# Kernel optimization log

Hardware: AMD Instinct MI355X
Metric: run time of the kernel (lower is better)

The kernel has to match this reference:

```python
import jax, jax.numpy as jnp
import numpy as np

LOG_2PI = float(np.log(2.0 * np.pi))
EPS = 1e-18


def setup_inputs() -> dict:
    key = jax.random.key(0)
    k1, k2, k3 = jax.random.split(key, 3)
    N_U, N_L, NZ = 4096, 65536, 32
    return {
        "pred": jax.random.normal(k1, (N_U,), dtype=jnp.float32),
        "U_z": jax.random.normal(k2, (N_U, NZ), dtype=jnp.float32),
        "L_z": jax.random.normal(k3, (N_L, NZ), dtype=jnp.float32),
    }


def reference(pred, U_z, L_z):
    # pred is accepted but unused by the original forward.
    nz = U_z.shape[1]
    # density: standard multivariate normal log-prob, mean 0, cov I
    dens = -0.5 * jnp.sum(U_z * U_z, axis=-1) - 0.5 * nz * LOG_2PI  # [N_U]
    # diversity: min_{z' in L_z} ||z - z'||_2 for each row of U_z
    # squared-distance expansion: ||u||^2 + ||l||^2 - 2 u.l
    u_sq = jnp.sum(U_z * U_z, axis=1)[:, None]        # [N_U, 1]
    l_sq = jnp.sum(L_z * L_z, axis=1)[None, :]        # [1, N_L]
    sq = u_sq + l_sq - 2.0 * (U_z @ L_z.T)            # [N_U, N_L]
    dists = jnp.sqrt(jnp.maximum(sq, 0.0))
    div = jnp.min(dists, axis=1)                      # [N_U]
    dd = jnp.exp(dens + jnp.log(div + EPS))
    dd = dd - jnp.min(dd)
    dd = dd / (jnp.max(dd) + EPS)
    return dd
```

## Files before the change

### kernel.cpp

```cpp
#include <hip/hip_runtime.h>
#include <hip/hip_bf16.h>

typedef _Float16 half8 __attribute__((ext_vector_type(8)));
typedef float f32x4 __attribute__((ext_vector_type(4)));
typedef unsigned int u32x4 __attribute__((ext_vector_type(4)));

#define N_U      4096
#define N_L      65536
#define NZ       32
#define NSPLIT   256
#define LSLICE   (N_L / NSPLIT)
#define NT       (LSLICE / 16)
#define UT       16
#define BM       1024
#define GY       (N_U / BM)

#define OFF_P1   0
#define OFF_USQ  (16 * 1024)
#define OFF_LF   (32 * 1024)
#define OFF_LSQ  (OFF_LF + N_L * NZ * 2)
#define OFF_UF   (OFF_LSQ + N_L * 4)

__device__ __forceinline__ unsigned int f2key(float f) {
    unsigned int u = __float_as_uint(f);
    return (u & 0x80000000u) ? ~u : (u | 0x80000000u);
}
__device__ __forceinline__ float key2f(unsigned int k) {
    unsigned int u = (k & 0x80000000u) ? (k & 0x7FFFFFFFu) : ~k;
    return __uint_as_float(u);
}

__global__ __launch_bounds__(256) void kPre(const float* __restrict__ Uz,
                                            const float* __restrict__ Lz,
                                            _Float16* __restrict__ Lf16,
                                            float* __restrict__ lsqh,
                                            _Float16* __restrict__ Uf16,
                                            float* __restrict__ usq,
                                            unsigned int* __restrict__ P1key) {
    int r = blockIdx.x * 256 + threadIdx.x;
    if (r < N_L) {
        const f32x4* src = (const f32x4*)(Lz + (size_t)r * NZ);
        _Float16* dst = Lf16 + (size_t)r * NZ;
        float s = 0.f;
#pragma unroll
        for (int j = 0; j < 4; ++j) {
            f32x4 a = src[2 * j], b = src[2 * j + 1];
            s = fmaf(a[0], a[0], s); s = fmaf(a[1], a[1], s);
            s = fmaf(a[2], a[2], s); s = fmaf(a[3], a[3], s);
            s = fmaf(b[0], b[0], s); s = fmaf(b[1], b[1], s);
            s = fmaf(b[2], b[2], s); s = fmaf(b[3], b[3], s);
            *(half8*)(dst + j * 8) =
                (half8){(_Float16)a[0], (_Float16)a[1], (_Float16)a[2], (_Float16)a[3],
                        (_Float16)b[0], (_Float16)b[1], (_Float16)b[2], (_Float16)b[3]};
        }
        lsqh[r] = -0.5f * s;
    } else if (r < N_L + N_U) {
        int u = r - N_L;
        const f32x4* src = (const f32x4*)(Uz + (size_t)u * NZ);
        _Float16* dst = Uf16 + (size_t)u * NZ;
        float s = 0.f;
#pragma unroll
        for (int j = 0; j < 4; ++j) {
            f32x4 a = src[2 * j], b = src[2 * j + 1];
            s = fmaf(a[0], a[0], s); s = fmaf(a[1], a[1], s);
            s = fmaf(a[2], a[2], s); s = fmaf(a[3], a[3], s);
            s = fmaf(b[0], b[0], s); s = fmaf(b[1], b[1], s);
            s = fmaf(b[2], b[2], s); s = fmaf(b[3], b[3], s);
            *(half8*)(dst + j * 8) =
                (half8){(_Float16)a[0], (_Float16)a[1], (_Float16)a[2], (_Float16)a[3],
                        (_Float16)b[0], (_Float16)b[1], (_Float16)b[2], (_Float16)b[3]};
        }
        usq[u] = s;
        P1key[u] = 0u;
    }
}

__global__ __launch_bounds__(256)
__attribute__((amdgpu_waves_per_eu(4, 4)))
void kA(const _Float16* __restrict__ Lf16,
        const float* __restrict__ lsqh,
        const _Float16* __restrict__ Uf16,
        unsigned int* __restrict__ P1key) {
    __shared__ __align__(16) unsigned char sm[LSLICE * 64 + LSLICE * 4];
    float* slsq = (float*)(sm + LSLICE * 64);

    const int tid  = threadIdx.x;
    const int lane = tid & 63;
    const int wave = tid >> 6;
    const int g    = lane >> 4;
    const int lc   = lane & 15;

    const int ubase = blockIdx.y * BM + wave * (UT * 16);
    const int lbase = blockIdx.x * LSLICE;

    {
        const half8* src = (const half8*)(Lf16 + (size_t)(lbase + tid) * NZ);
        unsigned char* dst = sm + ((tid >> 4) * 1024) + ((tid & 15) * 16);
#pragma unroll
        for (int j = 0; j < 4; ++j)
            *(half8*)(dst + j * 256) = src[j];
        slsq[tid] = lsqh[lbase + tid];
    }

    half8 bfrag[UT];
#pragma unroll
    for (int t = 0; t < UT; ++t)
        bfrag[t] = *(const half8*)(Uf16 + (size_t)(ubase + t * 16 + lc) * NZ + g * 8);
#pragma unroll
    for (int t = 0; t < UT; ++t)
        asm volatile("" : "+v"(bfrag[t]));

    float m[UT];
#pragma unroll
    for (int t = 0; t < UT; ++t) m[t] = -INFINITY;

    __syncthreads();

    const unsigned char* abase = sm + lane * 16;

#pragma unroll 2
    for (int lt = 0; lt < NT; ++lt) {
        const int pt = (lt + wave * 4) & (NT - 1);
        half8 a = *(const half8*)(abase + pt * 1024);
        f32x4 c = *(const f32x4*)(slsq + pt * 16 + g * 4);
#pragma unroll
        for (int t = 0; t < UT; ++t) {
            f32x4 x = __builtin_amdgcn_mfma_f32_16x16x32_f16(a, bfrag[t], c, 0, 0, 0);
            asm volatile("" : "+v"(x));
            float y = fmaxf(fmaxf(x[0], x[1]), x[2]);
            m[t] = fmaxf(fmaxf(y, x[3]), m[t]);
        }
    }

#pragma unroll
    for (int t = 0; t < UT; ++t) {
        float v = m[t];
        v = fmaxf(v, __shfl_xor(v, 16));
        v = fmaxf(v, __shfl_xor(v, 32));
        if (g == 0)
            atomicMax(&P1key[ubase + t * 16 + lc], f2key(v));
    }
}

__global__ __launch_bounds__(1024) void kB(const unsigned int* __restrict__ P1key,
                                           const float* __restrict__ usq,
                                           float* __restrict__ out) {
    const int t    = threadIdx.x;
    const int lane = t & 63;
    const int wid  = t >> 6;

    u32x4 kv = ((const u32x4*)P1key)[t];
    f32x4 uq = ((const f32x4*)usq)[t];

    float dd[4], lmin = INFINITY, lmax = -INFINITY;
#pragma unroll
    for (int j = 0; j < 4; ++j) {
        float M   = key2f(kv[j]);
        float sq  = fmaxf(fmaf(-2.f, M, uq[j]), 0.f);
        float dens = -0.5f * uq[j] - 29.406033062549525f;
        dd[j] = expf(dens) * (sqrtf(sq) + 1e-18f);
        lmin = fminf(lmin, dd[j]);
        lmax = fmaxf(lmax, dd[j]);
    }

    __shared__ float smn[16], smx[16];
#pragma unroll
    for (int o = 1; o < 64; o <<= 1) {
        lmin = fminf(lmin, __shfl_xor(lmin, o));
        lmax = fmaxf(lmax, __shfl_xor(lmax, o));
    }
    if (lane == 0) { smn[wid] = lmin; smx[wid] = lmax; }
    __syncthreads();
    if (wid == 0) {
        float a = (lane < 16) ? smn[lane] : INFINITY;
        float b = (lane < 16) ? smx[lane] : -INFINITY;
#pragma unroll
        for (int o = 1; o < 16; o <<= 1) {
            a = fminf(a, __shfl_xor(a, o));
            b = fmaxf(b, __shfl_xor(b, o));
        }
        if (lane == 0) { smn[0] = a; smx[0] = b; }
    }
    __syncthreads();
    float mn = smn[0], mx = smx[0];
    float inv = 1.f / ((mx - mn) + 1e-18f);

    f32x4 o4 = (f32x4){(dd[0] - mn) * inv, (dd[1] - mn) * inv,
                       (dd[2] - mn) * inv, (dd[3] - mn) * inv};
    ((f32x4*)out)[t] = o4;
}

extern "C" void kernel_launch(void* const* d_in, const int* in_sizes, int n_in,
                              void* d_out, int out_size, void* d_ws, size_t ws_size,
                              hipStream_t stream) {
    const float* Uz = (const float*)d_in[1];
    const float* Lz = (const float*)d_in[2];
    float* out = (float*)d_out;
    unsigned char* ws = (unsigned char*)d_ws;

    unsigned int* P1key = (unsigned int*)(ws + OFF_P1);
    float*        usq   = (float*)(ws + OFF_USQ);
    _Float16*     Lf16  = (_Float16*)(ws + OFF_LF);
    float*        lsqh  = (float*)(ws + OFF_LSQ);
    _Float16*     Uf16  = (_Float16*)(ws + OFF_UF);

    kPre<<<(N_L + N_U + 255) / 256, 256, 0, stream>>>(Uz, Lz, Lf16, lsqh, Uf16, usq, P1key);
    dim3 grid(NSPLIT, GY);
    kA<<<grid, 256, 0, stream>>>(Lf16, lsqh, Uf16, P1key);
    kB<<<1, 1024, 0, stream>>>(P1key, usq, out);
}
```

Measured before the change: 35.05 us.

## Fuse fp16 conversion and norm precompute into distance and finalize kernels

Removes the separate preprocessing kernel and performs the fp32-to-fp16 conversion and squared-norm computation of L rows inside the main MFMA kernel's shared-memory staging. U fragments are converted on load, and the finalize kernel recomputes U norms from the fp32 input. A memset replaces the key initialization. This saves one launch and the workspace round trip, in exchange for reading fp32 L from global memory in each of the 4 row-block groups and doing redundant conversion work.

```diff
diff --git a/kernel.cpp b/kernel.cpp
--- a/kernel.cpp
+++ b/kernel.cpp
@@ -16,10 +16,6 @@
 #define GY       (N_U / BM)
 
 #define OFF_P1   0
-#define OFF_USQ  (16 * 1024)
-#define OFF_LF   (32 * 1024)
-#define OFF_LSQ  (OFF_LF + N_L * NZ * 2)
-#define OFF_UF   (OFF_LSQ + N_L * 4)
 
 __device__ __forceinline__ unsigned int f2key(float f) {
     unsigned int u = __float_as_uint(f);
@@ -30,56 +26,10 @@
     return __uint_as_float(u);
 }
 
-__global__ __launch_bounds__(256) void kPre(const float* __restrict__ Uz,
-                                            const float* __restrict__ Lz,
-                                            _Float16* __restrict__ Lf16,
-                                            float* __restrict__ lsqh,
-                                            _Float16* __restrict__ Uf16,
-                                            float* __restrict__ usq,
-                                            unsigned int* __restrict__ P1key) {
-    int r = blockIdx.x * 256 + threadIdx.x;
-    if (r < N_L) {
-        const f32x4* src = (const f32x4*)(Lz + (size_t)r * NZ);
-        _Float16* dst = Lf16 + (size_t)r * NZ;
-        float s = 0.f;
-#pragma unroll
-        for (int j = 0; j < 4; ++j) {
-            f32x4 a = src[2 * j], b = src[2 * j + 1];
-            s = fmaf(a[0], a[0], s); s = fmaf(a[1], a[1], s);
-            s = fmaf(a[2], a[2], s); s = fmaf(a[3], a[3], s);
-            s = fmaf(b[0], b[0], s); s = fmaf(b[1], b[1], s);
-            s = fmaf(b[2], b[2], s); s = fmaf(b[3], b[3], s);
-            *(half8*)(dst + j * 8) =
-                (half8){(_Float16)a[0], (_Float16)a[1], (_Float16)a[2], (_Float16)a[3],
-                        (_Float16)b[0], (_Float16)b[1], (_Float16)b[2], (_Float16)b[3]};
-        }
-        lsqh[r] = -0.5f * s;
-    } else if (r < N_L + N_U) {
-        int u = r - N_L;
-        const f32x4* src = (const f32x4*)(Uz + (size_t)u * NZ);
-        _Float16* dst = Uf16 + (size_t)u * NZ;
-        float s = 0.f;
-#pragma unroll
-        for (int j = 0; j < 4; ++j) {
-            f32x4 a = src[2 * j], b = src[2 * j + 1];
-            s = fmaf(a[0], a[0], s); s = fmaf(a[1], a[1], s);
-            s = fmaf(a[2], a[2], s); s = fmaf(a[3], a[3], s);
-            s = fmaf(b[0], b[0], s); s = fmaf(b[1], b[1], s);
-            s = fmaf(b[2], b[2], s); s = fmaf(b[3], b[3], s);
-            *(half8*)(dst + j * 8) =
-                (half8){(_Float16)a[0], (_Float16)a[1], (_Float16)a[2], (_Float16)a[3],
-                        (_Float16)b[0], (_Float16)b[1], (_Float16)b[2], (_Float16)b[3]};
-        }
-        usq[u] = s;
-        P1key[u] = 0u;
-    }
-}
-
 __global__ __launch_bounds__(256)
 __attribute__((amdgpu_waves_per_eu(4, 4)))
-void kA(const _Float16* __restrict__ Lf16,
-        const float* __restrict__ lsqh,
-        const _Float16* __restrict__ Uf16,
+void kA(const float* __restrict__ Lz,
+        const float* __restrict__ Uz,
         unsigned int* __restrict__ P1key) {
     __shared__ __align__(16) unsigned char sm[LSLICE * 64 + LSLICE * 4];
     float* slsq = (float*)(sm + LSLICE * 64);
@@ -94,18 +44,31 @@
     const int lbase = blockIdx.x * LSLICE;
 
     {
-        const half8* src = (const half8*)(Lf16 + (size_t)(lbase + tid) * NZ);
+        const f32x4* src = (const f32x4*)(Lz + (size_t)(lbase + tid) * NZ);
         unsigned char* dst = sm + ((tid >> 4) * 1024) + ((tid & 15) * 16);
+        float s = 0.f;
 #pragma unroll
-        for (int j = 0; j < 4; ++j)
-            *(half8*)(dst + j * 256) = src[j];
-        slsq[tid] = lsqh[lbase + tid];
+        for (int j = 0; j < 4; ++j) {
+            f32x4 a = src[2 * j], b = src[2 * j + 1];
+            s = fmaf(a[0], a[0], s); s = fmaf(a[1], a[1], s);
+            s = fmaf(a[2], a[2], s); s = fmaf(a[3], a[3], s);
+            s = fmaf(b[0], b[0], s); s = fmaf(b[1], b[1], s);
+            s = fmaf(b[2], b[2], s); s = fmaf(b[3], b[3], s);
+            *(half8*)(dst + j * 256) =
+                (half8){(_Float16)a[0], (_Float16)a[1], (_Float16)a[2], (_Float16)a[3],
+                        (_Float16)b[0], (_Float16)b[1], (_Float16)b[2], (_Float16)b[3]};
+        }
+        slsq[tid] = -0.5f * s;
     }
 
     half8 bfrag[UT];
 #pragma unroll
-    for (int t = 0; t < UT; ++t)
-        bfrag[t] = *(const half8*)(Uf16 + (size_t)(ubase + t * 16 + lc) * NZ + g * 8);
+    for (int t = 0; t < UT; ++t) {
+        const f32x4* p = (const f32x4*)(Uz + (size_t)(ubase + t * 16 + lc) * NZ + g * 8);
+        f32x4 a = p[0], b = p[1];
+        bfrag[t] = (half8){(_Float16)a[0], (_Float16)a[1], (_Float16)a[2], (_Float16)a[3],
+                           (_Float16)b[0], (_Float16)b[1], (_Float16)b[2], (_Float16)b[3]};
+    }
 #pragma unroll
     for (int t = 0; t < UT; ++t)
         asm volatile("" : "+v"(bfrag[t]));
@@ -143,21 +106,29 @@
 }
 
 __global__ __launch_bounds__(1024) void kB(const unsigned int* __restrict__ P1key,
-                                           const float* __restrict__ usq,
+                                           const float* __restrict__ Uz,
                                            float* __restrict__ out) {
     const int t    = threadIdx.x;
     const int lane = t & 63;
     const int wid  = t >> 6;
 
     u32x4 kv = ((const u32x4*)P1key)[t];
-    f32x4 uq = ((const f32x4*)usq)[t];
 
     float dd[4], lmin = INFINITY, lmax = -INFINITY;
 #pragma unroll
     for (int j = 0; j < 4; ++j) {
+        const int u = t * 4 + j;
+        const f32x4* p = (const f32x4*)(Uz + (size_t)u * NZ);
+        float s = 0.f;
+#pragma unroll
+        for (int q = 0; q < 8; ++q) {
+            f32x4 v = p[q];
+            s = fmaf(v[0], v[0], s); s = fmaf(v[1], v[1], s);
+            s = fmaf(v[2], v[2], s); s = fmaf(v[3], v[3], s);
+        }
         float M   = key2f(kv[j]);
-        float sq  = fmaxf(fmaf(-2.f, M, uq[j]), 0.f);
-        float dens = -0.5f * uq[j] - 29.406033062549525f;
+        float sq  = fmaxf(fmaf(-2.f, M, s), 0.f);
+        float dens = -0.5f * s - 29.406033062549525f;
         dd[j] = expf(dens) * (sqrtf(sq) + 1e-18f);
         lmin = fminf(lmin, dd[j]);
         lmax = fmaxf(lmax, dd[j]);
@@ -199,13 +170,9 @@
     unsigned char* ws = (unsigned char*)d_ws;
 
     unsigned int* P1key = (unsigned int*)(ws + OFF_P1);
-    float*        usq   = (float*)(ws + OFF_USQ);
-    _Float16*     Lf16  = (_Float16*)(ws + OFF_LF);
-    float*        lsqh  = (float*)(ws + OFF_LSQ);
-    _Float16*     Uf16  = (_Float16*)(ws + OFF_UF);
 
-    kPre<<<(N_L + N_U + 255) / 256, 256, 0, stream>>>(Uz, Lz, Lf16, lsqh, Uf16, usq, P1key);
+    hipMemsetAsync(P1key, 0, N_U * sizeof(unsigned int), stream);
     dim3 grid(NSPLIT, GY);
-    kA<<<grid, 256, 0, stream>>>(Lf16, lsqh, Uf16, P1key);
-    kB<<<1, 1024, 0, stream>>>(P1key, usq, out);
+    kA<<<grid, 256, 0, stream>>>(Lz, Uz, P1key);
+    kB<<<1, 1024, 0, stream>>>(P1key, Uz, out);
 }
```

After: 59.70 us. 1.7x slower.
